# Optimization experiments

Measured on AMD Instinct MI355X. Metric: run time of the kernel, lower is better.

Reference implementation:

```python
import jax, jax.numpy as jnp
import numpy as np

N = 50000      # num nodes
E = 800000     # num edges
IN_C = 256
OUT_C = 128


def setup_inputs() -> dict:
    key = jax.random.key(0)
    k1, k2, k3, k4 = jax.random.split(key, 4)
    x = jax.random.normal(k1, (N, IN_C), dtype=jnp.float32)
    edge_index = jax.random.randint(k2, (2, E), 0, N, dtype=jnp.int64)
    # Linear params (Kaiming-uniform-ish scale like torch Linear reset)
    bound = 1.0 / np.sqrt(IN_C)
    W = jax.random.uniform(k3, (OUT_C, IN_C), minval=-bound, maxval=bound, dtype=jnp.float32)
    b = jax.random.uniform(k4, (OUT_C,), minval=-bound, maxval=bound, dtype=jnp.float32)
    return {"x": x, "edge_index": edge_index, "W": W, "b": b}


def reference(x, edge_index, W, b):
    # out = Linear(x): [N, OUT_C]
    out = jnp.einsum("ni,oi->no", x, W) + b
    src, dst = edge_index[0], edge_index[1]
    # gather source features: [E, OUT_C]
    src_feat = out[src]
    # scatter-mean by destination node
    summed = jax.ops.segment_sum(src_feat, dst, num_segments=N)  # [N, OUT_C]
    counts = jax.ops.segment_sum(jnp.ones((E,), dtype=out.dtype), dst, num_segments=N)
    mean = summed / jnp.maximum(counts, 1.0)[:, None]
    return mean
```

## Files before the change

kernel.cpp:

```cpp
#include <hip/hip_runtime.h>

#define N_NODES 50000
#define N_EDGES 800000
#define IN_CH   256
#define OUT_CH  128

#define NB        391
#define CAP       3072
#define L1_CHUNK  2048
#define GBM       64
#define NGEMM     ((N_NODES + GBM - 1) / GBM)

typedef __attribute__((ext_vector_type(8))) short short8;
typedef __attribute__((ext_vector_type(4))) float f32x4;

__device__ __forceinline__ short f2bf(float f) {
    unsigned u = __float_as_uint(f);
    unsigned r = (u + 0x7fffu + ((u >> 16) & 1u)) >> 16;
    return (short)r;
}

__global__ __launch_bounds__(256) void convert_w(const float* __restrict__ W,
                                                 short* __restrict__ Wbf,
                                                 int* __restrict__ bcnt) {
    int t = blockIdx.x * 256 + threadIdx.x;
    const float* wp = W + t * 8;
    float4 v0 = ((const float4*)wp)[0];
    float4 v1 = ((const float4*)wp)[1];
    short8 s;
    s[0]=f2bf(v0.x); s[1]=f2bf(v0.y); s[2]=f2bf(v0.z); s[3]=f2bf(v0.w);
    s[4]=f2bf(v1.x); s[5]=f2bf(v1.y); s[6]=f2bf(v1.z); s[7]=f2bf(v1.w);
    *(short8*)&Wbf[t * 8] = s;
    if (t < NB) bcnt[t] = 0;
}

#define GBK 32
#define LDK 40
__global__ __launch_bounds__(256) void gemm_bucket(const float* __restrict__ x,
                                                   const short* __restrict__ Wbf,
                                                   const float* __restrict__ bias,
                                                   short* __restrict__ linbf,
                                                   const int* __restrict__ src,
                                                   const int* __restrict__ dst,
                                                   int* __restrict__ bcnt,
                                                   unsigned* __restrict__ rec) {
    __shared__ __align__(16) char smem[15360];
    const int tid = threadIdx.x;

    if (blockIdx.x < NGEMM) {
        short* As = (short*)smem;
        short* Bs = (short*)(smem + 5120);

        const int m0  = blockIdx.x * GBM;
        const int w    = tid >> 6;
        const int lane = tid & 63;
        const int lm   = lane & 15;
        const int lq   = lane >> 4;
        const int wrow = (w >> 1) * 32;
        const int wcol = (w & 1) * 64;

        f32x4 acc[2][4];
#pragma unroll
        for (int i = 0; i < 2; ++i)
#pragma unroll
            for (int j = 0; j < 4; ++j) acc[i][j] = (f32x4)(0.0f);

        const int arow = tid >> 2;
        const int aq   = tid & 3;
        const int brow = tid >> 1;
        const int bhalf = tid & 1;

        for (int k0 = 0; k0 < IN_CH; k0 += GBK) {
            {
                float4 v0 = make_float4(0.f,0.f,0.f,0.f), v1 = v0;
                if (m0 + arow < N_NODES) {
                    const float* xp = x + (size_t)(m0 + arow) * IN_CH + k0 + aq * 8;
                    v0 = ((const float4*)xp)[0];
                    v1 = ((const float4*)xp)[1];
                }
                short8 s;
                s[0]=f2bf(v0.x); s[1]=f2bf(v0.y); s[2]=f2bf(v0.z); s[3]=f2bf(v0.w);
                s[4]=f2bf(v1.x); s[5]=f2bf(v1.y); s[6]=f2bf(v1.z); s[7]=f2bf(v1.w);
                *(short8*)&As[arow * LDK + aq * 8] = s;
            }
            {
                const short* wp = Wbf + (size_t)brow * IN_CH + k0 + bhalf * 16;
                *(short8*)&Bs[brow * LDK + bhalf * 16]     = ((const short8*)wp)[0];
                *(short8*)&Bs[brow * LDK + bhalf * 16 + 8] = ((const short8*)wp)[1];
            }
            __syncthreads();

            short8 af[2], bfr[4];
#pragma unroll
            for (int rt = 0; rt < 2; ++rt)
                af[rt] = *(const short8*)&As[(wrow + rt * 16 + lm) * LDK + lq * 8];
#pragma unroll
            for (int ct = 0; ct < 4; ++ct)
                bfr[ct] = *(const short8*)&Bs[(wcol + ct * 16 + lm) * LDK + lq * 8];
#pragma unroll
            for (int rt = 0; rt < 2; ++rt)
#pragma unroll
                for (int ct = 0; ct < 4; ++ct)
                    acc[rt][ct] = __builtin_amdgcn_mfma_f32_16x16x32_bf16(
                        af[rt], bfr[ct], acc[rt][ct], 0, 0, 0);
            __syncthreads();
        }

#pragma unroll
        for (int ct = 0; ct < 4; ++ct) {
            int gcol = wcol + ct * 16 + lm;
            float bv = bias[gcol];
#pragma unroll
            for (int rt = 0; rt < 2; ++rt) {
#pragma unroll
                for (int r = 0; r < 4; ++r) {
                    int grow = m0 + wrow + rt * 16 + lq * 4 + r;
                    if (grow < N_NODES)
                        linbf[(size_t)grow * OUT_CH + gcol] = f2bf(acc[rt][ct][r] + bv);
                }
            }
        }
    } else {
        int* lhist       = (int*)smem;
        int* lscan       = (int*)(smem + 1568);
        int* lbase       = (int*)(smem + 3136);
        unsigned* staged = (unsigned*)(smem + 4704);

        const int blk = blockIdx.x - NGEMM;
        const int e0  = blk * L1_CHUNK;
        const int total = min(L1_CHUNK, N_EDGES - e0);

        for (int i = tid; i < NB; i += 256) lhist[i] = 0;
        __syncthreads();

        unsigned mypk[8];
        int myr[8];
        int myb[8];
#pragma unroll
        for (int j = 0; j < 8; ++j) {
            int i = tid + j * 256;
            myb[j] = -1;
            if (i < total) {
                unsigned d = (unsigned)dst[e0 + i];
                unsigned s = (unsigned)src[e0 + i];
                int b = (int)(d >> 7);
                myb[j] = b;
                mypk[j] = s | ((d & 127u) << 16) | ((unsigned)b << 23);
                myr[j] = atomicAdd(&lhist[b], 1);
            }
        }
        __syncthreads();

        if (tid < 64) {
            int carry = 0;
            for (int c = 0; c < NB; c += 64) {
                int idx = c + tid;
                int v = (idx < NB) ? lhist[idx] : 0;
                int incl = v;
#pragma unroll
                for (int s = 1; s < 64; s <<= 1) {
                    int t = __shfl_up(incl, s, 64);
                    if (tid >= s) incl += t;
                }
                if (idx < NB) lscan[idx] = carry + incl - v;
                carry += __shfl(incl, 63, 64);
            }
        }
        __syncthreads();

        for (int bkt = tid; bkt < NB; bkt += 256) {
            int c = lhist[bkt];
            lbase[bkt] = c ? atomicAdd(&bcnt[bkt], c) : 0;
        }
#pragma unroll
        for (int j = 0; j < 8; ++j) {
            if (myb[j] >= 0)
                staged[lscan[myb[j]] + myr[j]] = mypk[j];
        }
        __syncthreads();

        for (int p = tid; p < total; p += 256) {
            unsigned r = staged[p];
            int b = (int)(r >> 23);
            int gpos = lbase[b] + (p - lscan[b]);
            if (gpos < CAP)
                rec[(size_t)b * CAP + gpos] = r;
        }
    }
}

#define FG_THR 1024
__global__ __launch_bounds__(FG_THR) void fine_gather(const int* __restrict__ bcnt,
                                                      const unsigned* __restrict__ rec,
                                                      const short* __restrict__ linbf,
                                                      float* __restrict__ out) {
    __shared__ unsigned srec[CAP];
    __shared__ unsigned short ssrc[CAP];
    __shared__ int fh[128], fo[128], fc[128];

    const int b = blockIdx.x;
    const int tid = threadIdx.x;
    const int cnt = min(bcnt[b], CAP);

    for (int i = tid; i < cnt; i += FG_THR)
        srec[i] = rec[(size_t)b * CAP + i];
    if (tid < 128) fh[tid] = 0;
    __syncthreads();

    for (int i = tid; i < cnt; i += FG_THR)
        atomicAdd(&fh[(srec[i] >> 16) & 127u], 1);
    __syncthreads();

    if (tid < 64) {
        int carry = 0;
        for (int c = 0; c < 128; c += 64) {
            int v = fh[c + tid];
            int incl = v;
#pragma unroll
            for (int s = 1; s < 64; s <<= 1) {
                int t = __shfl_up(incl, s, 64);
                if (tid >= s) incl += t;
            }
            fo[c + tid] = carry + incl - v;
            carry += __shfl(incl, 63, 64);
        }
    }
    __syncthreads();
    if (tid < 128) fc[tid] = fo[tid];
    __syncthreads();

    for (int i = tid; i < cnt; i += FG_THR) {
        unsigned r = srec[i];
        int p = atomicAdd(&fc[(r >> 16) & 127u], 1);
        ssrc[p] = (unsigned short)(r & 0xffffu);
    }
    __syncthreads();

    const int l = tid & 15;
#pragma unroll 1
    for (int g = 0; g < 2; ++g) {
        int nl = g * 64 + (tid >> 4);
        int n = b * 128 + nl;
        if (n >= N_NODES) continue;
        const int beg = fo[nl];
        const int deg = fh[nl];
        const int end = beg + deg;

        float a[8];
#pragma unroll
        for (int j = 0; j < 8; ++j) a[j] = 0.0f;

        int i = beg;
        for (; i + 3 < end; i += 4) {
            uint4 u[4];
#pragma unroll
            for (int e = 0; e < 4; ++e) {
                int s = ssrc[i + e];
                u[e] = *(const uint4*)&linbf[(size_t)s * OUT_CH + l * 8];
            }
#pragma unroll
            for (int e = 0; e < 4; ++e) {
                const unsigned* p = (const unsigned*)&u[e];
#pragma unroll
                for (int j = 0; j < 4; ++j) {
                    a[2*j]   += __uint_as_float(p[j] << 16);
                    a[2*j+1] += __uint_as_float(p[j] & 0xffff0000u);
                }
            }
        }
        for (; i < end; ++i) {
            int s = ssrc[i];
            uint4 u0 = *(const uint4*)&linbf[(size_t)s * OUT_CH + l * 8];
            const unsigned* p0 = (const unsigned*)&u0;
#pragma unroll
            for (int j = 0; j < 4; ++j) {
                a[2*j]   += __uint_as_float(p0[j] << 16);
                a[2*j+1] += __uint_as_float(p0[j] & 0xffff0000u);
            }
        }
        float inv = 1.0f / (float)(deg > 1 ? deg : 1);
        float4 o0, o1;
        o0.x = a[0]*inv; o0.y = a[1]*inv; o0.z = a[2]*inv; o0.w = a[3]*inv;
        o1.x = a[4]*inv; o1.y = a[5]*inv; o1.z = a[6]*inv; o1.w = a[7]*inv;
        float* op = &out[(size_t)n * OUT_CH + l * 8];
        ((float4*)op)[0] = o0;
        ((float4*)op)[1] = o1;
    }
}

extern "C" void kernel_launch(void* const* d_in, const int* in_sizes, int n_in,
                              void* d_out, int out_size, void* d_ws, size_t ws_size,
                              hipStream_t stream) {
    const float* x  = (const float*)d_in[0];
    const int*   ei = (const int*)d_in[1];
    const float* W  = (const float*)d_in[2];
    const float* b  = (const float*)d_in[3];
    float* out = (float*)d_out;

    const int* src = ei;
    const int* dst = ei + N_EDGES;

    char* ws = (char*)d_ws;
    short*    linbf = (short*)ws;    ws += ((size_t)N_NODES * OUT_CH * sizeof(short) + 255) & ~255ull;
    short*    Wbf   = (short*)ws;    ws += ((size_t)IN_CH * OUT_CH * sizeof(short) + 255) & ~255ull;
    unsigned* rec   = (unsigned*)ws; ws += ((size_t)NB * CAP * sizeof(unsigned) + 255) & ~255ull;
    int*      bcnt  = (int*)ws;

    convert_w<<<16, 256, 0, stream>>>(W, Wbf, bcnt);
    gemm_bucket<<<NGEMM + NB, 256, 0, stream>>>(x, Wbf, b, linbf, src, dst, bcnt, rec);
    fine_gather<<<NB, FG_THR, 0, stream>>>(bcnt, rec, linbf, out);
}
```

Before: 141.7 us.

## Split each fine_gather bucket across four 256-thread blocks by node quarter

Each 128-node bucket is now handled by four smaller blocks, each owning 32 destination nodes. Every block scans the whole bucket's records straight from global memory and keeps only those in its quarter, so shared memory per block shrinks and more blocks can run at once. The cost is that each block re-reads the full record list, four times the record traffic in total. The per-quarter source list is capped at 1024 entries, so a quarter holding more edges than that would lose them.

```diff
diff --git a/kernel.cpp b/kernel.cpp
--- a/kernel.cpp
+++ b/kernel.cpp
@@ -3,6 +3,8 @@
 #define N_NODES 50000
 #define N_EDGES 800000
 #define IN_CH   256
+#define OUT_C H_unused 0
+#undef OUT_C
 #define OUT_CH  128
 
 #define NB        391
@@ -189,61 +191,61 @@
     }
 }
 
-#define FG_THR 1024
+#define FG_THR 256
+#define QCAP   1024
 __global__ __launch_bounds__(FG_THR) void fine_gather(const int* __restrict__ bcnt,
                                                       const unsigned* __restrict__ rec,
                                                       const short* __restrict__ linbf,
                                                       float* __restrict__ out) {
-    __shared__ unsigned srec[CAP];
-    __shared__ unsigned short ssrc[CAP];
-    __shared__ int fh[128], fo[128], fc[128];
-
-    const int b = blockIdx.x;
+    __shared__ unsigned short ssrc[QCAP];
+    __shared__ int fh[32], fo[32], fc[32];
+
     const int tid = threadIdx.x;
+    const int b   = blockIdx.x >> 2;
+    const int q   = blockIdx.x & 3;
+    const int lo  = q * 32;
     const int cnt = min(bcnt[b], CAP);
-
-    for (int i = tid; i < cnt; i += FG_THR)
-        srec[i] = rec[(size_t)b * CAP + i];
-    if (tid < 128) fh[tid] = 0;
+    const unsigned* rp = rec + (size_t)b * CAP;
+
+    if (tid < 32) fh[tid] = 0;
     __syncthreads();
 
-    for (int i = tid; i < cnt; i += FG_THR)
-        atomicAdd(&fh[(srec[i] >> 16) & 127u], 1);
+    for (int i = tid; i < cnt; i += FG_THR) {
+        int f = (int)((rp[i] >> 16) & 127u) - lo;
+        if ((unsigned)f < 32u) atomicAdd(&fh[f], 1);
+    }
     __syncthreads();
 
-    if (tid < 64) {
-        int carry = 0;
-        for (int c = 0; c < 128; c += 64) {
-            int v = fh[c + tid];
-            int incl = v;
-#pragma unroll
-            for (int s = 1; s < 64; s <<= 1) {
-                int t = __shfl_up(incl, s, 64);
-                if (tid >= s) incl += t;
-            }
-            fo[c + tid] = carry + incl - v;
-            carry += __shfl(incl, 63, 64);
-        }
+    if (tid < 32) {
+        int v = fh[tid], incl = v;
+#pragma unroll
+        for (int s = 1; s < 32; s <<= 1) {
+            int t = __shfl_up(incl, s, 32);
+            if (tid >= s) incl += t;
+        }
+        fo[tid] = incl - v;
+        fc[tid] = incl - v;
     }
     __syncthreads();
-    if (tid < 128) fc[tid] = fo[tid];
-    __syncthreads();
 
     for (int i = tid; i < cnt; i += FG_THR) {
-        unsigned r = srec[i];
-        int p = atomicAdd(&fc[(r >> 16) & 127u], 1);
-        ssrc[p] = (unsigned short)(r & 0xffffu);
+        unsigned r = rp[i];
+        int f = (int)((r >> 16) & 127u) - lo;
+        if ((unsigned)f < 32u) {
+            int p = atomicAdd(&fc[f], 1);
+            if (p < QCAP) ssrc[p] = (unsigned short)(r & 0xffffu);
+        }
     }
     __syncthreads();
 
     const int l = tid & 15;
 #pragma unroll 1
     for (int g = 0; g < 2; ++g) {
-        int nl = g * 64 + (tid >> 4);
-        int n = b * 128 + nl;
+        int fn = g * 16 + (tid >> 4);
+        int n = b * 128 + lo + fn;
         if (n >= N_NODES) continue;
-        const int beg = fo[nl];
-        const int deg = fh[nl];
+        const int beg = fo[fn];
+        const int deg = fh[fn];
         const int end = beg + deg;
 
         float a[8];
@@ -308,5 +310,5 @@
 
     convert_w<<<16, 256, 0, stream>>>(W, Wbf, bcnt);
     gemm_bucket<<<NGEMM + NB, 256, 0, stream>>>(x, Wbf, b, linbf, src, dst, bcnt, rec);
-    fine_gather<<<NB, FG_THR, 0, stream>>>(bcnt, rec, linbf, out);
-}
+    fine_gather<<<NB * 4, FG_THR, 0, stream>>>(bcnt, rec, linbf, out);
+}
```

Result: slower. 145.4 us (+2.6%).
